# Kernel tuning notes

Hardware: AMD Instinct MI355X
Metric: run time of the kernel (lower is better)

## Reference

```python
import jax, jax.numpy as jnp
import numpy as np

DIM = 1024
DEPTH = 6
HEADS = 16
DH = 64
INNER = HEADS * DH  # 1024
MLP = 4096
B, N = 2, 2048
SCALE = DH ** (-0.5)  # 0.125; module divides softmax output by this (x8)
EPS = 1e-5


def setup_inputs() -> dict:
    key = jax.random.key(0)
    ks = jax.random.split(key, 5)
    s = jnp.float32(0.02)
    return {
        "x": jax.random.normal(ks[0], (B, N, DIM), dtype=jnp.float32),
        "ln1_g": jnp.ones((DEPTH, DIM), jnp.float32),
        "ln1_b": jnp.zeros((DEPTH, DIM), jnp.float32),
        "w_qkv": jax.random.normal(ks[1], (DEPTH, DIM, 3 * INNER), jnp.float32) * s,
        "w_out": jax.random.normal(ks[2], (DEPTH, INNER, DIM), jnp.float32) * s,
        "b_out": jnp.zeros((DEPTH, DIM), jnp.float32),
        "ln2_g": jnp.ones((DEPTH, DIM), jnp.float32),
        "ln2_b": jnp.zeros((DEPTH, DIM), jnp.float32),
        "w1": jax.random.normal(ks[3], (DEPTH, DIM, MLP), jnp.float32) * s,
        "b1": jnp.zeros((DEPTH, MLP), jnp.float32),
        "w2": jax.random.normal(ks[4], (DEPTH, MLP, DIM), jnp.float32) * s,
        "b2": jnp.zeros((DEPTH, DIM), jnp.float32),
    }


def _layernorm(x, g, b):
    m = x.mean(-1, keepdims=True)
    v = ((x - m) ** 2).mean(-1, keepdims=True)
    return (x - m) * jax.lax.rsqrt(v + EPS) * g + b


def _attention(x, w_qkv, w_out, b_out):
    b, n, _ = x.shape
    qkv = x @ w_qkv  # [b, n, 3*inner]
    q, k, v = jnp.split(qkv, 3, axis=-1)

    def heads(t):
        return t.reshape(b, n, HEADS, DH).transpose(0, 2, 1, 3)  # [b,h,n,d]

    q, k, v = heads(q), heads(k), heads(v)
    # Faithful to source: softmax of UNSCALED logits, then divide by scale.
    score = jax.nn.softmax(jnp.einsum("bhqd,bhkd->bhqk", q, k), axis=-1) / SCALE
    o = jnp.einsum("bhqk,bhkd->bhqd", score, v)
    o = o.transpose(0, 2, 1, 3).reshape(b, n, INNER)
    return o @ w_out + b_out


def reference(x, ln1_g, ln1_b, w_qkv, w_out, b_out, ln2_g, ln2_b, w1, b1, w2, b2):
    def layer(h, p):
        g1, bb1, wq, wo, bo, g2, bb2, ww1, bw1, ww2, bw2 = p
        h = h + _attention(_layernorm(h, g1, bb1), wq, wo, bo)
        f = _layernorm(h, g2, bb2) @ ww1 + bw1
        f = jax.nn.gelu(f, approximate=False)  # nn.GELU default = exact erf
        h = h + f @ ww2 + bw2
        return h, None

    out, _ = jax.lax.scan(
        layer, x, (ln1_g, ln1_b, w_qkv, w_out, b_out, ln2_g, ln2_b, w1, b1, w2, b2)
    )
    return out
```

## Files before the change

kernel.cpp:

```cpp
#include <hip/hip_runtime.h>
#include <cstdint>

typedef __attribute__((ext_vector_type(4))) float f32x4;
typedef __attribute__((ext_vector_type(8))) short short8;
typedef __attribute__((ext_vector_type(4))) short short4v;
typedef _Float16 half8v __attribute__((ext_vector_type(8)));

__device__ __forceinline__ unsigned short f2h(float x) {
  _Float16 h = (_Float16)x;
  return __builtin_bit_cast(unsigned short, h);
}
__device__ __forceinline__ unsigned int pk2(float a, float b) {
  auto h = __builtin_amdgcn_cvt_pkrtz(a, b);
  return __builtin_bit_cast(unsigned int, h);
}

template <typename V>
__device__ __forceinline__ auto mfma_impl(V a, V b, f32x4 c, int)
    -> decltype(__builtin_amdgcn_mfma_f32_16x16x32_f16(a, b, c, 0, 0, 0)) {
  return __builtin_amdgcn_mfma_f32_16x16x32_f16(a, b, c, 0, 0, 0);
}
template <typename V>
__device__ __forceinline__ f32x4 mfma_impl(V a, V b, f32x4 c, long) {
  return __builtin_amdgcn_mfma_f32_16x16x32_f16(
      __builtin_bit_cast(half8v, a), __builtin_bit_cast(half8v, b), c, 0, 0, 0);
}
__device__ __forceinline__ f32x4 MFMA(short8 a, short8 b, f32x4 c) {
  return mfma_impl(a, b, c, 0);
}

__device__ __forceinline__ void load_lds16(const void* g, void* l) {
  __builtin_amdgcn_global_load_lds(
      (__attribute__((address_space(1))) void*)(uintptr_t)g,
      (__attribute__((address_space(3))) void*)l, 16, 0, 0);
}

__global__ __launch_bounds__(256) void ln_f16_kernel(
    const float* __restrict__ X, const float* __restrict__ gam,
    const float* __restrict__ bet, unsigned short* __restrict__ Y) {
  __shared__ float red[8];
  const int row = blockIdx.x, t = threadIdx.x;
  const float4 v = ((const float4*)(X + (size_t)row * 1024))[t];
  float s = v.x + v.y + v.z + v.w;
#pragma unroll
  for (int o = 32; o >= 1; o >>= 1) s += __shfl_xor(s, o, 64);
  if ((t & 63) == 0) red[t >> 6] = s;
  __syncthreads();
  const float mean = (red[0] + red[1] + red[2] + red[3]) * (1.0f / 1024.0f);
  const float dx = v.x - mean, dy = v.y - mean, dz = v.z - mean, dw = v.w - mean;
  float ss = dx * dx + dy * dy + dz * dz + dw * dw;
#pragma unroll
  for (int o = 32; o >= 1; o >>= 1) ss += __shfl_xor(ss, o, 64);
  if ((t & 63) == 0) red[4 + (t >> 6)] = ss;
  __syncthreads();
  const float var = (red[4] + red[5] + red[6] + red[7]) * (1.0f / 1024.0f);
  const float rstd = rsqrtf(var + 1e-5f);
  const float4 gg = ((const float4*)gam)[t];
  const float4 bb = ((const float4*)bet)[t];
  ushort4 o4;
  o4.x = f2h(dx * rstd * gg.x + bb.x);
  o4.y = f2h(dy * rstd * gg.y + bb.y);
  o4.z = f2h(dz * rstd * gg.z + bb.z);
  o4.w = f2h(dw * rstd * gg.w + bb.w);
  ((ushort4*)(Y + (size_t)row * 1024))[t] = o4;
}

__global__ __launch_bounds__(256) void transpose_f16_kernel(
    const float* __restrict__ W, unsigned short* __restrict__ WT, int K, int N) {
  __shared__ float t[32][33];
  const int n0 = blockIdx.x * 32, k0 = blockIdx.y * 32;
  const int tx = threadIdx.x, ty = threadIdx.y;
#pragma unroll
  for (int i = 0; i < 4; ++i)
    t[ty + 8 * i][tx] = W[(size_t)(k0 + ty + 8 * i) * N + n0 + tx];
  __syncthreads();
#pragma unroll
  for (int i = 0; i < 4; ++i)
    WT[(size_t)(n0 + ty + 8 * i) * K + k0 + tx] = f2h(t[tx][ty + 8 * i]);
}

template <int BM, int EPI>
__global__ __launch_bounds__(256, BM == 64 ? 3 : 2) void gemm_f16_kernel(
    const unsigned short* __restrict__ A, const unsigned short* __restrict__ BT,
    void* Cout, const float* __restrict__ bias, const float* __restrict__ res,
    int M, int N, int K) {
  constexpr int BN = 128, BK = 64;
  constexpr int MR = BM / 32;
  constexpr int ACH = BM * BK / 8;
  constexpr int BCH = BN * BK / 8;
  __shared__ alignas(16) unsigned short a_sh[2][BM * BK];
  __shared__ alignas(16) unsigned short b_sh[2][BN * BK];
  const int tid = threadIdx.x;
  const int w = tid >> 6, lane = tid & 63, g = lane >> 4, lm = lane & 15;
  const int m0 = blockIdx.y * BM, n0 = blockIdx.x * BN;
  const int wm = (w >> 1) * (BM / 2), wn = (w & 1) * 64;
  f32x4 acc[MR][4] = {};
  const int nsteps = K >> 6;

  auto stage = [&](int buf, int kk) {
#pragma unroll
    for (int c0 = 0; c0 < ACH; c0 += 256) {
      const int c = c0 + tid, row = c >> 3;
      const int sc = (c & 7) ^ (row & 7);
      const int cb = c0 + (tid & 192);
      load_lds16(A + (size_t)(m0 + row) * K + kk + sc * 8, &a_sh[buf][cb * 8]);
    }
#pragma unroll
    for (int c0 = 0; c0 < BCH; c0 += 256) {
      const int c = c0 + tid, row = c >> 3;
      const int sc = (c & 7) ^ (row & 7);
      const int cb = c0 + (tid & 192);
      load_lds16(BT + (size_t)(n0 + row) * K + kk + sc * 8, &b_sh[buf][cb * 8]);
    }
  };

  stage(0, 0);
  __syncthreads();
  int cur = 0;
  for (int step = 0; step < nsteps; ++step) {
    if (step + 1 < nsteps) stage(cur ^ 1, (step + 1) * BK);
#pragma unroll
    for (int kc = 0; kc < 2; ++kc) {
      short8 af[MR], bfr[4];
#pragma unroll
      for (int i = 0; i < MR; ++i) {
        const int r = wm + i * 16 + lm;
        af[i] = *(const short8*)&a_sh[cur][r * 64 + (((kc << 2) | g) ^ (r & 7)) * 8];
      }
#pragma unroll
      for (int j = 0; j < 4; ++j) {
        const int r = wn + j * 16 + lm;
        bfr[j] = *(const short8*)&b_sh[cur][r * 64 + (((kc << 2) | g) ^ (r & 7)) * 8];
      }
#pragma unroll
      for (int i = 0; i < MR; ++i)
#pragma unroll
        for (int j = 0; j < 4; ++j)
          acc[i][j] = MFMA(af[i], bfr[j], acc[i][j]);
    }
    if (step + 1 < nsteps) {
      __syncthreads();
      cur ^= 1;
    }
  }

#pragma unroll
  for (int i = 0; i < MR; ++i) {
    const int row = m0 + wm + i * 16 + g * 4;
#pragma unroll
    for (int j = 0; j < 4; ++j) {
      const int col = n0 + wn + j * 16 + lm;
#pragma unroll
      for (int r = 0; r < 4; ++r) {
        const float v = acc[i][j][r];
        const size_t idx = (size_t)(row + r) * N + col;
        if (EPI == 0) {
          ((unsigned short*)Cout)[idx] = f2h(v);
        } else if (EPI == 1) {
          const float xx = v + bias[col];
          ((unsigned short*)Cout)[idx] =
              f2h(0.5f * xx * (1.0f + erff(xx * 0.70710678118654752f)));
        } else {
          ((float*)Cout)[idx] = res[idx] + v + bias[col];
        }
      }
    }
  }
}

__global__ __launch_bounds__(256) void attn_kernel(
    const unsigned short* __restrict__ qkv, unsigned short* __restrict__ obuf) {
  constexpr int PK = 72;
  constexpr int PV = 68;
  __shared__ alignas(16) unsigned short Qs[64 * PK];
  __shared__ alignas(16) unsigned short Ks[64 * PK];
  __shared__ alignas(16) unsigned short VsT[64 * PV];
  const int tid = threadIdx.x;
  const int w = tid >> 6, lane = tid & 63, g = lane >> 4, lm = lane & 15;
  const int qbase = blockIdx.x * 64, h = blockIdx.y, b = blockIdx.z;
  const size_t rowbase = (size_t)b * 2048;
  const int r0 = tid >> 3, cc = tid & 7;

  const unsigned short* qptr = qkv + (rowbase + qbase + r0) * 3072 + h * 64 + cc * 8;
#pragma unroll
  for (int s = 0; s < 2; ++s)
    *(uint4*)&Qs[(s * 32 + r0) * PK + cc * 8] = *(const uint4*)(qptr + (size_t)s * 32 * 3072);

  const unsigned short* kvptr = qkv + (rowbase + r0) * 3072 + h * 64 + cc * 8;
  uint4 kreg[2], vreg[2];
#pragma unroll
  for (int s = 0; s < 2; ++s) {
    kreg[s] = *(const uint4*)(kvptr + 1024 + (size_t)s * 32 * 3072);
    vreg[s] = *(const uint4*)(kvptr + 2048 + (size_t)s * 32 * 3072);
  }
  __syncthreads();
  short8 qf[2];
#pragma unroll
  for (int s2 = 0; s2 < 2; ++s2)
    qf[s2] = *(const short8*)&Qs[(w * 16 + lm) * PK + s2 * 32 + g * 8];

  float mrun = -1e30f, lrun = 0.0f;
  f32x4 accO[4] = {};
  const int kdst = r0 * PK + cc * 8;

  for (int kv0 = 0; kv0 < 2048; kv0 += 64) {
    __syncthreads();
#pragma unroll
    for (int s = 0; s < 2; ++s) {
      *(uint4*)&Ks[kdst + s * 32 * PK] = kreg[s];
      const unsigned* vu = (const unsigned*)&vreg[s];
#pragma unroll
      for (int e2 = 0; e2 < 4; ++e2) {
        const unsigned v2 = vu[e2];
        VsT[(cc * 8 + 2 * e2) * PV + 32 * s + r0] = (unsigned short)(v2 & 0xffffu);
        VsT[(cc * 8 + 2 * e2 + 1) * PV + 32 * s + r0] = (unsigned short)(v2 >> 16);
      }
    }
    __syncthreads();
    if (kv0 + 64 < 2048) {
      const unsigned short* np = kvptr + (size_t)(kv0 + 64) * 3072;
#pragma unroll
      for (int s = 0; s < 2; ++s) {
        kreg[s] = *(const uint4*)(np + 1024 + (size_t)s * 32 * 3072);
        vreg[s] = *(const uint4*)(np + 2048 + (size_t)s * 32 * 3072);
      }
    }

    f32x4 sf[4] = {};
#pragma unroll
    for (int s2 = 0; s2 < 2; ++s2)
#pragma unroll
      for (int i = 0; i < 4; ++i) {
        const short8 kf = *(const short8*)&Ks[(i * 16 + lm) * PK + s2 * 32 + g * 8];
        sf[i] = MFMA(kf, qf[s2], sf[i]);
      }

    float tmax = -1e30f;
#pragma unroll
    for (int i = 0; i < 4; ++i)
#pragma unroll
      for (int r = 0; r < 4; ++r) tmax = fmaxf(tmax, sf[i][r]);
    tmax = fmaxf(tmax, __shfl_xor(tmax, 16, 64));
    tmax = fmaxf(tmax, __shfl_xor(tmax, 32, 64));
    const float mnew = fmaxf(mrun, tmax);
    const float scale = __expf(mrun - mnew);
    float p[4][4];
    float psum = 0.0f;
#pragma unroll
    for (int i = 0; i < 4; ++i)
#pragma unroll
      for (int r = 0; r < 4; ++r) {
        p[i][r] = __expf(sf[i][r] - mnew);
        psum += p[i][r];
      }
    psum += __shfl_xor(psum, 16, 64);
    psum += __shfl_xor(psum, 32, 64);
    lrun = lrun * scale + psum;
    mrun = mnew;
#pragma unroll
    for (int t = 0; t < 4; ++t) accO[t] = accO[t] * scale;

    uint4 pbu[2];
#pragma unroll
    for (int blk = 0; blk < 2; ++blk) {
      pbu[blk].x = pk2(p[2 * blk][0], p[2 * blk][1]);
      pbu[blk].y = pk2(p[2 * blk][2], p[2 * blk][3]);
      pbu[blk].z = pk2(p[2 * blk + 1][0], p[2 * blk + 1][1]);
      pbu[blk].w = pk2(p[2 * blk + 1][2], p[2 * blk + 1][3]);
    }

#pragma unroll
    for (int blk = 0; blk < 2; ++blk) {
      const short8 pbv = __builtin_bit_cast(short8, pbu[blk]);
#pragma unroll
      for (int t = 0; t < 4; ++t) {
        const int base = (16 * t + lm) * PV + 32 * blk + 4 * g;
        const short4v vlo = *(const short4v*)&VsT[base];
        const short4v vhi = *(const short4v*)&VsT[base + 16];
        const short8 vf = {vlo[0], vlo[1], vlo[2], vlo[3],
                           vhi[0], vhi[1], vhi[2], vhi[3]};
        accO[t] = MFMA(vf, pbv, accO[t]);
      }
    }
  }

  const float inv = 8.0f / lrun;
  const size_t orow = rowbase + qbase + w * 16 + lm;
#pragma unroll
  for (int t = 0; t < 4; ++t)
#pragma unroll
    for (int r = 0; r < 4; ++r) {
      const int col = h * 64 + t * 16 + g * 4 + r;
      obuf[orow * 1024 + col] = f2h(accO[t][r] * inv);
    }
}

extern "C" void kernel_launch(void* const* d_in, const int* in_sizes, int n_in,
                              void* d_out, int out_size, void* d_ws, size_t ws_size,
                              hipStream_t stream) {
  const float* x     = (const float*)d_in[0];
  const float* ln1_g = (const float*)d_in[1];
  const float* ln1_b = (const float*)d_in[2];
  const float* w_qkv = (const float*)d_in[3];
  const float* w_out = (const float*)d_in[4];
  const float* b_out = (const float*)d_in[5];
  const float* ln2_g = (const float*)d_in[6];
  const float* ln2_b = (const float*)d_in[7];
  const float* w1    = (const float*)d_in[8];
  const float* b1    = (const float*)d_in[9];
  const float* w2    = (const float*)d_in[10];
  const float* b2    = (const float*)d_in[11];
  float* h = (float*)d_out;

  char* ws = (char*)d_ws;
  const size_t MB = 1u << 20;
  unsigned short* xn   = (unsigned short*)(ws);
  unsigned short* ob   = (unsigned short*)(ws + 8 * MB);
  unsigned short* qkvb = (unsigned short*)(ws + 16 * MB);
  unsigned short* mid  = (unsigned short*)(ws + 40 * MB);
  unsigned short* wt   = (unsigned short*)(ws + 72 * MB);

  hipError_t e0 = hipMemcpyAsync(h, x, (size_t)4096 * 1024 * sizeof(float),
                                 hipMemcpyDeviceToDevice, stream);
  (void)e0;

  const dim3 tb(32, 8);
  for (int L = 0; L < 6; ++L) {
    const float* Lg1 = ln1_g + L * 1024;
    const float* Lb1 = ln1_b + L * 1024;
    const float* Lwq = w_qkv + (size_t)L * 1024 * 3072;
    const float* Lwo = w_out + (size_t)L * 1024 * 1024;
    const float* Lbo = b_out + L * 1024;
    const float* Lg2 = ln2_g + L * 1024;
    const float* Lb2 = ln2_b + L * 1024;
    const float* Lw1 = w1 + (size_t)L * 1024 * 4096;
    const float* Lb1m = b1 + L * 4096;
    const float* Lw2 = w2 + (size_t)L * 4096 * 1024;
    const float* Lb2m = b2 + L * 1024;

    ln_f16_kernel<<<4096, 256, 0, stream>>>(h, Lg1, Lb1, xn);
    transpose_f16_kernel<<<dim3(96, 32), tb, 0, stream>>>(Lwq, wt, 1024, 3072);
    gemm_f16_kernel<128, 0><<<dim3(24, 32), 256, 0, stream>>>(
        xn, wt, qkvb, nullptr, nullptr, 4096, 3072, 1024);
    attn_kernel<<<dim3(32, 16, 2), 256, 0, stream>>>(qkvb, ob);
    transpose_f16_kernel<<<dim3(32, 32), tb, 0, stream>>>(Lwo, wt, 1024, 1024);
    gemm_f16_kernel<64, 2><<<dim3(8, 64), 256, 0, stream>>>(
        ob, wt, h, Lbo, h, 4096, 1024, 1024);

    ln_f16_kernel<<<4096, 256, 0, stream>>>(h, Lg2, Lb2, xn);
    transpose_f16_kernel<<<dim3(128, 32), tb, 0, stream>>>(Lw1, wt, 1024, 4096);
    gemm_f16_kernel<128, 1><<<dim3(32, 32), 256, 0, stream>>>(
        xn, wt, mid, Lb1m, nullptr, 4096, 4096, 1024);
    transpose_f16_kernel<<<dim3(32, 128), tb, 0, stream>>>(Lw2, wt, 4096, 1024);
    gemm_f16_kernel<64, 2><<<dim3(8, 64), 256, 0, stream>>>(
        mid, wt, h, Lb2m, h, 4096, 1024, 4096);
  }
  (void)in_sizes; (void)n_in; (void)out_size; (void)ws_size;
}
```

Before: 1.830 ms.

## Double-buffer K/V tiles in attention kernel with one barrier per iteration

Attention K/V shared-memory tiles become double-buffered, so the next tile is written to the alternate buffer while the current one is consumed. This cuts the per-iteration barriers from two to one and prefetches global loads two tiles ahead. The MFMA sections are wrapped in s_setprio hints, and output stores are vectorised to 4-element writes. The cost is doubled LDS use for K/V, which may lower occupancy.

```diff
diff --git a/kernel.cpp b/kernel.cpp
--- a/kernel.cpp
+++ b/kernel.cpp
@@ -173,13 +173,14 @@
   constexpr int PK = 72;
   constexpr int PV = 68;
   __shared__ alignas(16) unsigned short Qs[64 * PK];
-  __shared__ alignas(16) unsigned short Ks[64 * PK];
-  __shared__ alignas(16) unsigned short VsT[64 * PV];
+  __shared__ alignas(16) unsigned short Ks[2][64 * PK];
+  __shared__ alignas(16) unsigned short VsT[2][64 * PV];
   const int tid = threadIdx.x;
   const int w = tid >> 6, lane = tid & 63, g = lane >> 4, lm = lane & 15;
   const int qbase = blockIdx.x * 64, h = blockIdx.y, b = blockIdx.z;
   const size_t rowbase = (size_t)b * 2048;
   const int r0 = tid >> 3, cc = tid & 7;
+  const int kdst = r0 * PK + cc * 8;
 
   const unsigned short* qptr = qkv + (rowbase + qbase + r0) * 3072 + h * 64 + cc * 8;
 #pragma unroll
@@ -188,11 +189,32 @@
 
   const unsigned short* kvptr = qkv + (rowbase + r0) * 3072 + h * 64 + cc * 8;
   uint4 kreg[2], vreg[2];
-#pragma unroll
-  for (int s = 0; s < 2; ++s) {
-    kreg[s] = *(const uint4*)(kvptr + 1024 + (size_t)s * 32 * 3072);
-    vreg[s] = *(const uint4*)(kvptr + 2048 + (size_t)s * 32 * 3072);
-  }
+
+  auto load_tile = [&](int n) {
+    const unsigned short* np = kvptr + (size_t)n * 64 * 3072;
+#pragma unroll
+    for (int s = 0; s < 2; ++s) {
+      kreg[s] = *(const uint4*)(np + 1024 + (size_t)s * 32 * 3072);
+      vreg[s] = *(const uint4*)(np + 2048 + (size_t)s * 32 * 3072);
+    }
+  };
+  auto write_tile = [&](int buf) {
+#pragma unroll
+    for (int s = 0; s < 2; ++s) {
+      *(uint4*)&Ks[buf][kdst + s * 32 * PK] = kreg[s];
+      const unsigned* vu = (const unsigned*)&vreg[s];
+#pragma unroll
+      for (int e2 = 0; e2 < 4; ++e2) {
+        const unsigned v2 = vu[e2];
+        VsT[buf][(cc * 8 + 2 * e2) * PV + 32 * s + r0] = (unsigned short)(v2 & 0xffffu);
+        VsT[buf][(cc * 8 + 2 * e2 + 1) * PV + 32 * s + r0] = (unsigned short)(v2 >> 16);
+      }
+    }
+  };
+
+  load_tile(0);
+  write_tile(0);
+  load_tile(1);
   __syncthreads();
   short8 qf[2];
 #pragma unroll
@@ -201,39 +223,25 @@
 
   float mrun = -1e30f, lrun = 0.0f;
   f32x4 accO[4] = {};
-  const int kdst = r0 * PK + cc * 8;
-
-  for (int kv0 = 0; kv0 < 2048; kv0 += 64) {
-    __syncthreads();
-#pragma unroll
-    for (int s = 0; s < 2; ++s) {
-      *(uint4*)&Ks[kdst + s * 32 * PK] = kreg[s];
-      const unsigned* vu = (const unsigned*)&vreg[s];
-#pragma unroll
-      for (int e2 = 0; e2 < 4; ++e2) {
-        const unsigned v2 = vu[e2];
-        VsT[(cc * 8 + 2 * e2) * PV + 32 * s + r0] = (unsigned short)(v2 & 0xffffu);
-        VsT[(cc * 8 + 2 * e2 + 1) * PV + 32 * s + r0] = (unsigned short)(v2 >> 16);
-      }
-    }
-    __syncthreads();
-    if (kv0 + 64 < 2048) {
-      const unsigned short* np = kvptr + (size_t)(kv0 + 64) * 3072;
-#pragma unroll
-      for (int s = 0; s < 2; ++s) {
-        kreg[s] = *(const uint4*)(np + 1024 + (size_t)s * 32 * 3072);
-        vreg[s] = *(const uint4*)(np + 2048 + (size_t)s * 32 * 3072);
-      }
+
+  for (int n = 0; n < 32; ++n) {
+    const int cur = n & 1;
+    if (n) __syncthreads();
+    if (n + 1 < 32) {
+      write_tile(cur ^ 1);
+      if (n + 2 < 32) load_tile(n + 2);
     }
 
     f32x4 sf[4] = {};
+    __builtin_amdgcn_s_setprio(1);
 #pragma unroll
     for (int s2 = 0; s2 < 2; ++s2)
 #pragma unroll
       for (int i = 0; i < 4; ++i) {
-        const short8 kf = *(const short8*)&Ks[(i * 16 + lm) * PK + s2 * 32 + g * 8];
+        const short8 kf = *(const short8*)&Ks[cur][(i * 16 + lm) * PK + s2 * 32 + g * 8];
         sf[i] = MFMA(kf, qf[s2], sf[i]);
       }
+    __builtin_amdgcn_s_setprio(0);
 
     float tmax = -1e30f;
 #pragma unroll
@@ -269,30 +277,34 @@
       pbu[blk].w = pk2(p[2 * blk + 1][2], p[2 * blk + 1][3]);
     }
 
+    __builtin_amdgcn_s_setprio(1);
 #pragma unroll
     for (int blk = 0; blk < 2; ++blk) {
       const short8 pbv = __builtin_bit_cast(short8, pbu[blk]);
 #pragma unroll
       for (int t = 0; t < 4; ++t) {
         const int base = (16 * t + lm) * PV + 32 * blk + 4 * g;
-        const short4v vlo = *(const short4v*)&VsT[base];
-        const short4v vhi = *(const short4v*)&VsT[base + 16];
+        const short4v vlo = *(const short4v*)&VsT[cur][base];
+        const short4v vhi = *(const short4v*)&VsT[cur][base + 16];
         const short8 vf = {vlo[0], vlo[1], vlo[2], vlo[3],
                            vhi[0], vhi[1], vhi[2], vhi[3]};
         accO[t] = MFMA(vf, pbv, accO[t]);
       }
     }
+    __builtin_amdgcn_s_setprio(0);
   }
 
   const float inv = 8.0f / lrun;
   const size_t orow = rowbase + qbase + w * 16 + lm;
 #pragma unroll
-  for (int t = 0; t < 4; ++t)
-#pragma unroll
-    for (int r = 0; r < 4; ++r) {
-      const int col = h * 64 + t * 16 + g * 4 + r;
-      obuf[orow * 1024 + col] = f2h(accO[t][r] * inv);
-    }
+  for (int t = 0; t < 4; ++t) {
+    ushort4 o4;
+    o4.x = f2h(accO[t][0] * inv);
+    o4.y = f2h(accO[t][1] * inv);
+    o4.z = f2h(accO[t][2] * inv);
+    o4.w = f2h(accO[t][3] * inv);
+    *(ushort4*)&obuf[orow * 1024 + h * 64 + t * 16 + g * 4] = o4;
+  }
 }
 
 extern "C" void kernel_launch(void* const* d_in, const int* in_sizes, int n_in,
```

Measured after the change: 1.975 ms. 1.08x slower.
